# Performance work log

Hardware: AMD Instinct MI355X
Metric: run time of the kernel (lower is better)

## Reference

```python
import jax, jax.numpy as jnp
import numpy as np

NUM_IN_CH = 64
DIM = 256
HEADS = 8


def conv1x1(x, w):
    # x: [b,c,h,w], w: [o,c,1,1] -> [b,o,h,w]
    return jnp.einsum('bchw,oc->bohw', x, w[:, :, 0, 0])


def dwconv3(x, w):
    # depthwise 3x3, padding=1; w: [c,1,3,3]
    return jax.lax.conv_general_dilated(
        x, w, window_strides=(1, 1), padding='SAME',
        feature_group_count=x.shape[1],
        dimension_numbers=('NCHW', 'OIHW', 'NCHW'))


def setup_inputs() -> dict:
    key = jax.random.key(0)
    ks = jax.random.split(key, 12)
    B, C, H, W = 8, NUM_IN_CH, 128, 128
    s = 0.02
    return {
        'x': jax.random.normal(ks[0], (B, C, H, W), jnp.float32),
        'y': jax.random.normal(ks[1], (B, C, H, W), jnp.float32),
        'z': jax.random.normal(ks[2], (B, C, H, W), jnp.float32),
        'Wq': jax.random.normal(ks[3], (DIM, C, 1, 1), jnp.float32) * s,
        'Wq_dw': jax.random.normal(ks[4], (DIM, 1, 3, 3), jnp.float32) * s,
        'Wk': jax.random.normal(ks[5], (DIM, C, 1, 1), jnp.float32) * s,
        'Wk_dw': jax.random.normal(ks[6], (DIM, 1, 3, 3), jnp.float32) * s,
        'Wv': jax.random.normal(ks[7], (DIM, C, 1, 1), jnp.float32) * s,
        'Wv_dw': jax.random.normal(ks[8], (DIM, 1, 3, 3), jnp.float32) * s,
        'Wproj': jax.random.normal(ks[9], (DIM, DIM, 1, 1), jnp.float32) * s,
        'Wfus': jax.random.normal(ks[10], (DIM, 3 * C, 1, 1), jnp.float32) * s,
        'temperature': jnp.ones((HEADS, 1, 1), jnp.float32),
    }


def reference(x, y, z, Wq, Wq_dw, Wk, Wk_dw, Wv, Wv_dw, Wproj, Wfus, temperature):
    b, c, h, w = x.shape
    hw = h * w
    q = dwconv3(conv1x1(x, Wq), Wq_dw)
    k = dwconv3(conv1x1(y, Wk), Wk_dw)
    v = dwconv3(conv1x1(z, Wv), Wv_dw)
    f = conv1x1(jnp.concatenate([x, y, z], axis=1), Wfus)

    def to_heads(t):  # [b, dim, h, w] -> [b, head, c_head, hw]
        return t.reshape(b, HEADS, DIM // HEADS, hw)

    q, k, v = to_heads(q), to_heads(k), to_heads(v)
    # L2-normalize over the spatial (hw) axis, eps matches torch F.normalize
    qn = q / jnp.maximum(jnp.sqrt(jnp.sum(q * q, axis=-1, keepdims=True)), 1e-12)
    kn = k / jnp.maximum(jnp.sqrt(jnp.sum(k * k, axis=-1, keepdims=True)), 1e-12)
    attn = jnp.einsum('bhcn,bhdn->bhcd', qn, kn) * temperature  # [b,head,c,c]
    attn = jax.nn.softmax(attn, axis=-1)
    out = jnp.einsum('bhcd,bhdn->bhcn', attn, v).reshape(b, DIM, h, w)
    out = conv1x1(out, Wproj)
    return out + f
```

## Files before the change

kernel.cpp:

```cpp
#include <hip/hip_runtime.h>
#include <cstdint>

#define B_   8
#define CIN  64
#define DIM_ 256
#define H_   128
#define W_   128
#define HW_  (H_*W_)

typedef unsigned short u16;
typedef unsigned int   u32;
typedef short short8 __attribute__((ext_vector_type(8)));
typedef float f32x4  __attribute__((ext_vector_type(4)));

__device__ __forceinline__ u16 f2bf(float f) {
    u32 u = __float_as_uint(f);
    u32 r = (u + 0x7fffu + ((u >> 16) & 1u)) >> 16;
    return (u16)r;
}
__device__ __forceinline__ float bf2f(u16 h) {
    return __uint_as_float(((u32)h) << 16);
}

__global__ __launch_bounds__(256) void conv_mfma_kernel(
    const float* __restrict__ in, const float* __restrict__ Wc,
    u16* __restrict__ pre)
{
    __shared__ u16 Alds[256 * 64];
    __shared__ u16 Blds[128 * 64];

    const int tid = threadIdx.x;
    const int b = blockIdx.y;
    const int px0 = blockIdx.x * 128;

    {
        const int row = tid;
        const float* wp = Wc + (size_t)row * 64;
        #pragma unroll
        for (int s = 0; s < 8; ++s) {
            float4 f0 = *(const float4*)(wp + s * 8);
            float4 f1 = *(const float4*)(wp + s * 8 + 4);
            uint4 pk;
            pk.x = f2bf(f0.x) | ((u32)f2bf(f0.y) << 16);
            pk.y = f2bf(f0.z) | ((u32)f2bf(f0.w) << 16);
            pk.z = f2bf(f1.x) | ((u32)f2bf(f1.y) << 16);
            pk.w = f2bf(f1.z) | ((u32)f2bf(f1.w) << 16);
            *(uint4*)&Alds[row * 64 + ((s * 8) ^ ((row & 7) << 3))] = pk;
        }
    }
    #pragma unroll
    for (int v4 = 0; v4 < 4; ++v4) {
        int it = tid + v4 * 256;
        int px = it & 127, cg = it >> 7;
        const float* sp = in + ((size_t)b * CIN + cg * 8) * HW_ + px0 + px;
        u32 wv[4];
        #pragma unroll
        for (int j = 0; j < 4; ++j) {
            float a = sp[(size_t)(2 * j) * HW_];
            float c = sp[(size_t)(2 * j + 1) * HW_];
            wv[j] = f2bf(a) | ((u32)f2bf(c) << 16);
        }
        *(uint4*)&Blds[px * 64 + ((cg * 8) ^ ((px & 7) << 3))] =
            make_uint4(wv[0], wv[1], wv[2], wv[3]);
    }
    __syncthreads();

    const int lane = tid & 63, wid = tid >> 6;
    const int g = lane >> 4, ln = lane & 15;
    const int m0 = wid * 64;
    f32x4 acc[4][8] = {};

    #pragma unroll
    for (int ks = 0; ks < 2; ++ks) {
        short8 af[4];
        #pragma unroll
        for (int fm = 0; fm < 4; ++fm) {
            int m = m0 + fm * 16 + ln;
            af[fm] = *(const short8*)&Alds[m * 64 + ((ks * 32 + g * 8) ^ ((m & 7) << 3))];
        }
        #pragma unroll
        for (int fn = 0; fn < 8; ++fn) {
            int p = fn * 16 + ln;
            short8 bf = *(const short8*)&Blds[p * 64 + ((ks * 32 + g * 8) ^ ((p & 7) << 3))];
            #pragma unroll
            for (int fm = 0; fm < 4; ++fm)
                acc[fm][fn] = __builtin_amdgcn_mfma_f32_16x16x32_bf16(af[fm], bf, acc[fm][fn], 0, 0, 0);
        }
    }

    u16* op = pre + (size_t)b * DIM_ * HW_;
    #pragma unroll
    for (int fm = 0; fm < 4; ++fm)
        #pragma unroll
        for (int fn = 0; fn < 8; ++fn)
            #pragma unroll
            for (int r = 0; r < 4; ++r) {
                int ch = m0 + fm * 16 + g * 4 + r;
                op[(size_t)ch * HW_ + px0 + fn * 16 + ln] = f2bf(acc[fm][fn][r]);
            }
}

__global__ __launch_bounds__(256) void dw_kernel(
    const u16* __restrict__ pre, const float* __restrict__ Wd,
    u16* __restrict__ dst)
{
    __shared__ u16 t0[34][144];

    const int tid = threadIdx.x;
    const int y0 = blockIdx.x * 32;
    const int ch = blockIdx.y;
    const int b = blockIdx.z;
    const u16* src = pre + ((size_t)b * DIM_ + ch) * HW_;

    for (int i = tid; i < 68; i += 256)
        t0[i >> 1][(i & 1) ? 136 : 7] = 0;
    for (int i = tid; i < 544; i += 256) {
        int row = i >> 4, seg = i & 15;
        int gy = y0 - 1 + row;
        uint4 v = make_uint4(0, 0, 0, 0);
        if (gy >= 0 && gy < H_) v = *(const uint4*)(src + (size_t)gy * W_ + seg * 8);
        *(uint4*)&t0[row][8 + seg * 8] = v;
    }
    const float* wv = Wd + (size_t)ch * 9;
    float w00 = wv[0], w01 = wv[1], w02 = wv[2];
    float w10 = wv[3], w11 = wv[4], w12 = wv[5];
    float w20 = wv[6], w21 = wv[7], w22 = wv[8];
    __syncthreads();

    const int px = tid & 127, half = tid >> 7;
    u16* op = dst + ((size_t)b * DIM_ + ch) * HW_;
    float h0m2 = 0.f, h0m1 = 0.f, h1m1 = 0.f;
    #pragma unroll
    for (int y = 0; y < 18; ++y) {
        int r = half * 16 + y;
        float v0 = bf2f(t0[r][7 + px]);
        float v1 = bf2f(t0[r][8 + px]);
        float v2 = bf2f(t0[r][9 + px]);
        float h0 = fmaf(v0, w00, fmaf(v1, w01, v2 * w02));
        float h1 = fmaf(v0, w10, fmaf(v1, w11, v2 * w12));
        float h2 = fmaf(v0, w20, fmaf(v1, w21, v2 * w22));
        if (y >= 2)
            op[(size_t)(y0 + half * 16 + y - 2) * W_ + px] = f2bf(h0m2 + h1m1 + h2);
        h0m2 = h0m1; h0m1 = h0; h1m1 = h1;
    }
}

__global__ __launch_bounds__(256) void gram_mfma_kernel(
    const u16* __restrict__ q, const u16* __restrict__ k,
    float* __restrict__ pgram, float* __restrict__ pssq, float* __restrict__ pssk)
{
    __shared__ float red[4][1024];
    __shared__ float redq[4][32];
    __shared__ float redk[4][32];

    const int bh = blockIdx.y;
    const int chunk = blockIdx.x;
    const int tid = threadIdx.x;
    const int lane = tid & 63, wid = tid >> 6;
    const int g = lane >> 4, ln = lane & 15;

    const size_t off = (size_t)(bh * 32 + ln) * HW_ + chunk * 2048 + wid * 512 + g * 8;
    const u16* qp = q + off;
    const u16* kp = k + off;

    f32x4 aqk[2][2] = {};
    f32x4 aqq[2] = {};
    f32x4 akk[2] = {};

    #pragma unroll 4
    for (int n = 0; n < 512; n += 32) {
        short8 qf[2], kf[2];
        qf[0] = *(const short8*)(qp + n);
        qf[1] = *(const short8*)(qp + (size_t)16 * HW_ + n);
        kf[0] = *(const short8*)(kp + n);
        kf[1] = *(const short8*)(kp + (size_t)16 * HW_ + n);
        #pragma unroll
        for (int ti = 0; ti < 2; ++ti)
            #pragma unroll
            for (int tj = 0; tj < 2; ++tj)
                aqk[ti][tj] = __builtin_amdgcn_mfma_f32_16x16x32_bf16(qf[ti], kf[tj], aqk[ti][tj], 0, 0, 0);
        #pragma unroll
        for (int ti = 0; ti < 2; ++ti) {
            aqq[ti] = __builtin_amdgcn_mfma_f32_16x16x32_bf16(qf[ti], qf[ti], aqq[ti], 0, 0, 0);
            akk[ti] = __builtin_amdgcn_mfma_f32_16x16x32_bf16(kf[ti], kf[ti], akk[ti], 0, 0, 0);
        }
    }

    #pragma unroll
    for (int ti = 0; ti < 2; ++ti)
        #pragma unroll
        for (int tj = 0; tj < 2; ++tj)
            #pragma unroll
            for (int r = 0; r < 4; ++r)
                red[wid][(ti * 16 + g * 4 + r) * 32 + tj * 16 + ln] = aqk[ti][tj][r];
    if ((ln >> 2) == g) {
        #pragma unroll
        for (int ti = 0; ti < 2; ++ti) {
            redq[wid][ti * 16 + ln] = aqq[ti][ln & 3];
            redk[wid][ti * 16 + ln] = akk[ti][ln & 3];
        }
    }
    __syncthreads();

    for (int p = tid; p < 1024; p += 256) {
        float s = red[0][p] + red[1][p] + red[2][p] + red[3][p];
        pgram[((size_t)bh * 8 + chunk) * 1024 + p] = s;
    }
    if (tid < 32) {
        pssq[((size_t)bh * 8 + chunk) * 32 + tid] =
            redq[0][tid] + redq[1][tid] + redq[2][tid] + redq[3][tid];
    } else if (tid < 64) {
        int j = tid & 31;
        pssk[((size_t)bh * 8 + chunk) * 32 + j] =
            redk[0][j] + redk[1][j] + redk[2][j] + redk[3][j];
    }
}

__global__ __launch_bounds__(256) void softproj_kernel(
    const float* __restrict__ pgram, const float* __restrict__ pssq,
    const float* __restrict__ pssk, const float* __restrict__ Wproj,
    const float* __restrict__ temp, u16* __restrict__ Amm)
{
    __shared__ float att[32][33];
    __shared__ float nq[32], nk[32];

    const int bh = blockIdx.x;
    const int h = bh & 7;
    const int b = bh >> 3;
    const int tid = threadIdx.x;

    for (int p = tid; p < 1024; p += 256) {
        float s = 0.f;
        #pragma unroll
        for (int c = 0; c < 8; ++c) s += pgram[((size_t)bh * 8 + c) * 1024 + p];
        att[p >> 5][p & 31] = s;
    }
    if (tid < 32) {
        float s = 0.f;
        #pragma unroll
        for (int c = 0; c < 8; ++c) s += pssq[((size_t)bh * 8 + c) * 32 + tid];
        nq[tid] = fmaxf(sqrtf(s), 1e-12f);
    } else if (tid < 64) {
        int i = tid & 31;
        float s = 0.f;
        #pragma unroll
        for (int c = 0; c < 8; ++c) s += pssk[((size_t)bh * 8 + c) * 32 + i];
        nk[i] = fmaxf(sqrtf(s), 1e-12f);
    }
    __syncthreads();

    const float T = temp[h];
    if (tid < 32) {
        int i = tid;
        float row[32];
        float mx = -1e30f;
        float qi = T / nq[i];
        #pragma unroll
        for (int j = 0; j < 32; ++j) {
            float v = att[i][j] * qi / nk[j];
            row[j] = v;
            mx = fmaxf(mx, v);
        }
        float s = 0.f;
        #pragma unroll
        for (int j = 0; j < 32; ++j) { float e = expf(row[j] - mx); row[j] = e; s += e; }
        float inv = 1.f / s;
        #pragma unroll
        for (int j = 0; j < 32; ++j) att[i][j] = row[j] * inv;
    }
    __syncthreads();

    const int o = tid;
    float wp[32];
    #pragma unroll
    for (int i2 = 0; i2 < 32; i2 += 4)
        *(float4*)&wp[i2] = *(const float4*)&Wproj[(size_t)o * DIM_ + h * 32 + i2];
    u16* arow = Amm + ((size_t)b * DIM_ + o) * DIM_ + h * 32;
    #pragma unroll
    for (int j = 0; j < 32; ++j) {
        float s = 0.f;
        #pragma unroll
        for (int i = 0; i < 32; ++i) s = fmaf(wp[i], att[i][j], s);
        arow[j] = f2bf(s);
    }
}

__global__ __launch_bounds__(256) void wfus_cast_kernel(
    const float* __restrict__ Wfus, u16* __restrict__ Afus)
{
    int idx = blockIdx.x * 256 + threadIdx.x;
    int base = idx * 8;
    float4 f0 = *(const float4*)(Wfus + base);
    float4 f1 = *(const float4*)(Wfus + base + 4);
    uint4 pk;
    pk.x = f2bf(f0.x) | ((u32)f2bf(f0.y) << 16);
    pk.y = f2bf(f0.z) | ((u32)f2bf(f0.w) << 16);
    pk.z = f2bf(f1.x) | ((u32)f2bf(f1.y) << 16);
    pk.w = f2bf(f1.z) | ((u32)f2bf(f1.w) << 16);
    *(uint4*)(Afus + base) = pk;
}

#define LOADB_F4(KC, W) do {                                                    \
    if ((KC) < 4) {                                                             \
        _Pragma("unroll") for (int i_ = 0; i_ < 2; ++i_) {                      \
            const u16* vb_ = vbuf + ((size_t)b * DIM_ + (KC) * 64 + (qq0 + 2 * i_) * 16) * HW_ + px0 + pxu; \
            _Pragma("unroll") for (int jj_ = 0; jj_ < 8; ++jj_)                 \
                W[i_][jj_] = (u32)vb_[(size_t)(2 * jj_) * HW_]                  \
                           | ((u32)vb_[(size_t)(2 * jj_ + 1) * HW_] << 16);     \
        }                                                                       \
    } else {                                                                    \
        const float* bp_ = ((KC) == 4) ? xin : ((KC) == 5) ? yin : zin;         \
        _Pragma("unroll") for (int i_ = 0; i_ < 2; ++i_) {                      \
            const float* sp_ = bp_ + ((size_t)b * CIN + (qq0 + 2 * i_) * 16) * HW_ + px0 + pxu; \
            _Pragma("unroll") for (int jj_ = 0; jj_ < 8; ++jj_)                 \
                W[i_][jj_] = (u32)f2bf(sp_[(size_t)(2 * jj_) * HW_])            \
                           | ((u32)f2bf(sp_[(size_t)(2 * jj_ + 1) * HW_]) << 16); \
        }                                                                       \
    } } while (0)

#define WRITEB_F4(BUF, W) do {                                                  \
    u16* dd_ = &Bl[BUF][pxu * 64];                                              \
    _Pragma("unroll") for (int i_ = 0; i_ < 2; ++i_) {                          \
        int qq_ = qq0 + 2 * i_;                                                 \
        *(uint4*)&dd_[(qq_ * 16)     ^ ((pxu & 7) << 3)] = make_uint4(W[i_][0], W[i_][1], W[i_][2], W[i_][3]); \
        *(uint4*)&dd_[(qq_ * 16 + 8) ^ ((pxu & 7) << 3)] = make_uint4(W[i_][4], W[i_][5], W[i_][6], W[i_][7]); \
    } } while (0)

#define LOADA_F4(KC, A) do {                                                    \
    _Pragma("unroll") for (int ks_ = 0; ks_ < 2; ++ks_)                         \
    _Pragma("unroll") for (int fm_ = 0; fm_ < 2; ++fm_) {                       \
        int m_ = m0 + fm_ * 16 + ln;                                            \
        const u16* ap_ = ((KC) < 4)                                             \
            ? Amm + ((size_t)b * DIM_ + m_) * DIM_ + (KC) * 64 + ks_ * 32 + g * 8 \
            : Afus + (size_t)m_ * 192 + ((KC) - 4) * 64 + ks_ * 32 + g * 8;     \
        A[ks_ * 2 + fm_] = *(const short8*)ap_;                                 \
    } } while (0)

__global__ __launch_bounds__(256) void final4_kernel(
    const u16* __restrict__ Amm, const u16* __restrict__ Afus,
    const u16* __restrict__ vbuf,
    const float* __restrict__ xin, const float* __restrict__ yin,
    const float* __restrict__ zin, float* __restrict__ out)
{
    __shared__ u16 Bl[2][128 * 64];

    const int tid = threadIdx.x;
    const int px0 = blockIdx.x * 128;
    const int o0  = blockIdx.y * 128;
    const int b   = blockIdx.z;
    const int lane = tid & 63, wid = tid >> 6;
    const int g = lane >> 4, ln = lane & 15;
    const int m0 = o0 + wid * 32;
    const int pxu = tid & 127;
    const int qq0 = tid >> 7;

    f32x4 acc[2][8] = {};
    short8 aC[4], aN[4];
    u32 wN[2][8];

    LOADA_F4(0, aC);
    {
        u32 w0[2][8];
        LOADB_F4(0, w0);
        WRITEB_F4(0, w0);
    }
    __syncthreads();
    LOADA_F4(1, aN);
    LOADB_F4(1, wN);

    #pragma unroll
    for (int kc = 0; kc < 7; ++kc) {
        const int cur = kc & 1;

        #pragma unroll
        for (int ks = 0; ks < 2; ++ks)
            #pragma unroll
            for (int fn = 0; fn < 8; ++fn) {
                int p = fn * 16 + ln;
                short8 bf = *(const short8*)&Bl[cur][p * 64 + ((ks * 32 + g * 8) ^ ((p & 7) << 3))];
                acc[0][fn] = __builtin_amdgcn_mfma_f32_16x16x32_bf16(aC[ks * 2 + 0], bf, acc[0][fn], 0, 0, 0);
                acc[1][fn] = __builtin_amdgcn_mfma_f32_16x16x32_bf16(aC[ks * 2 + 1], bf, acc[1][fn], 0, 0, 0);
            }

        if (kc < 6) {
            WRITEB_F4(cur ^ 1, wN);
            __syncthreads();
            #pragma unroll
            for (int r = 0; r < 4; ++r) aC[r] = aN[r];
            if (kc < 5) {
                LOADA_F4(kc + 2, aN);
                LOADB_F4(kc + 2, wN);
            }
        }
    }

    float* op = out + (size_t)b * DIM_ * HW_;
    #pragma unroll
    for (int fm = 0; fm < 2; ++fm)
        #pragma unroll
        for (int fn = 0; fn < 8; ++fn)
            #pragma unroll
            for (int r = 0; r < 4; ++r) {
                int ch = m0 + fm * 16 + g * 4 + r;
                op[(size_t)ch * HW_ + px0 + fn * 16 + ln] = acc[fm][fn][r];
            }
}

extern "C" void kernel_launch(void* const* d_in, const int* in_sizes, int n_in,
                              void* d_out, int out_size, void* d_ws, size_t ws_size,
                              hipStream_t stream) {
    (void)in_sizes; (void)n_in; (void)out_size; (void)ws_size;

    const float* x     = (const float*)d_in[0];
    const float* y     = (const float*)d_in[1];
    const float* z     = (const float*)d_in[2];
    const float* Wq    = (const float*)d_in[3];
    const float* Wqd   = (const float*)d_in[4];
    const float* Wk    = (const float*)d_in[5];
    const float* Wkd   = (const float*)d_in[6];
    const float* Wv    = (const float*)d_in[7];
    const float* Wvd   = (const float*)d_in[8];
    const float* Wproj = (const float*)d_in[9];
    const float* Wfus  = (const float*)d_in[10];
    const float* temp  = (const float*)d_in[11];

    const size_t QELEMS = (size_t)B_ * DIM_ * HW_;

    u16* preb = (u16*)d_out;
    u16* qbuf = (u16*)d_out + QELEMS;
    u16* kvbuf = (u16*)d_ws;
    char* wsp = (char*)d_ws + QELEMS * sizeof(u16);
    float* pgram = (float*)wsp;                       wsp += 64 * 8 * 1024 * 4;
    float* pssq  = (float*)wsp;                       wsp += 64 * 8 * 32 * 4;
    float* pssk  = (float*)wsp;                       wsp += 64 * 8 * 32 * 4;
    u16*   Amm   = (u16*)wsp;                         wsp += (size_t)B_ * DIM_ * DIM_ * 2;
    u16*   Afus  = (u16*)wsp;

    dim3 cgrid(128, B_);
    dim3 dgrid(4, DIM_, B_);

    wfus_cast_kernel<<<24, 256, 0, stream>>>(Wfus, Afus);
    conv_mfma_kernel<<<cgrid, 256, 0, stream>>>(x, Wq, preb);
    dw_kernel<<<dgrid, 256, 0, stream>>>(preb, Wqd, qbuf);
    conv_mfma_kernel<<<cgrid, 256, 0, stream>>>(y, Wk, preb);
    dw_kernel<<<dgrid, 256, 0, stream>>>(preb, Wkd, kvbuf);
    gram_mfma_kernel<<<dim3(8, 64), 256, 0, stream>>>(qbuf, kvbuf, pgram, pssq, pssk);
    softproj_kernel<<<64, 256, 0, stream>>>(pgram, pssq, pssk, Wproj, temp, Amm);
    conv_mfma_kernel<<<cgrid, 256, 0, stream>>>(z, Wv, preb);
    dw_kernel<<<dgrid, 256, 0, stream>>>(preb, Wvd, kvbuf);
    final4_kernel<<<dim3(128, 2, B_), 256, 0, stream>>>(Amm, Afus, kvbuf, x, y, z, (float*)d_out);
}
```

Baseline: 289.8 us.

## Store V path in pixel-major layout so final GEMM reads B fragments directly

Adds a V 1x1 conv kernel that transposes its output through LDS into pixel-major (channel-contiguous) layout. It also adds a depthwise conv kernel that works on that layout with vectorized channel loads. The final GEMM then loads the V operand fragments straight from global memory as short8 vectors, instead of gathering strided bf16 values and staging them in LDS. This is meant to remove uncoalesced 2-byte gathers. The cost is an extra LDS transpose pass and a dwconv that re-reads neighbours from global memory without LDS tiling.

```diff
diff --git a/kernel.cpp b/kernel.cpp
--- a/kernel.cpp
+++ b/kernel.cpp
@@ -98,6 +98,100 @@
                 int ch = m0 + fm * 16 + g * 4 + r;
                 op[(size_t)ch * HW_ + px0 + fn * 16 + ln] = f2bf(acc[fm][fn][r]);
             }
+}
+
+__global__ __launch_bounds__(256) void conv_mfma_t_kernel(
+    const float* __restrict__ in, const float* __restrict__ Wc,
+    u16* __restrict__ preT)
+{
+    __shared__ u16 S[128 * 264];
+
+    u16* Alds = S;
+    u16* Blds = S + 16384;
+
+    const int tid = threadIdx.x;
+    const int b = blockIdx.y;
+    const int px0 = blockIdx.x * 128;
+
+    {
+        const int row = tid;
+        const float* wp = Wc + (size_t)row * 64;
+        #pragma unroll
+        for (int s = 0; s < 8; ++s) {
+            float4 f0 = *(const float4*)(wp + s * 8);
+            float4 f1 = *(const float4*)(wp + s * 8 + 4);
+            uint4 pk;
+            pk.x = f2bf(f0.x) | ((u32)f2bf(f0.y) << 16);
+            pk.y = f2bf(f0.z) | ((u32)f2bf(f0.w) << 16);
+            pk.z = f2bf(f1.x) | ((u32)f2bf(f1.y) << 16);
+            pk.w = f2bf(f1.z) | ((u32)f2bf(f1.w) << 16);
+            *(uint4*)&Alds[row * 64 + ((s * 8) ^ ((row & 7) << 3))] = pk;
+        }
+    }
+    #pragma unroll
+    for (int v4 = 0; v4 < 4; ++v4) {
+        int it = tid + v4 * 256;
+        int px = it & 127, cg = it >> 7;
+        const float* sp = in + ((size_t)b * CIN + cg * 8) * HW_ + px0 + px;
+        u32 wv[4];
+        #pragma unroll
+        for (int j = 0; j < 4; ++j) {
+            float a = sp[(size_t)(2 * j) * HW_];
+            float c = sp[(size_t)(2 * j + 1) * HW_];
+            wv[j] = f2bf(a) | ((u32)f2bf(c) << 16);
+        }
+        *(uint4*)&Blds[px * 64 + ((cg * 8) ^ ((px & 7) << 3))] =
+            make_uint4(wv[0], wv[1], wv[2], wv[3]);
+    }
+    __syncthreads();
+
+    const int lane = tid & 63, wid = tid >> 6;
+    const int g = lane >> 4, ln = lane & 15;
+    const int m0 = wid * 64;
+    f32x4 acc[4][8] = {};
+
+    #pragma unroll
+    for (int ks = 0; ks < 2; ++ks) {
+        short8 af[4];
+        #pragma unroll
+        for (int fm = 0; fm < 4; ++fm) {
+            int m = m0 + fm * 16 + ln;
+            af[fm] = *(const short8*)&Alds[m * 64 + ((ks * 32 + g * 8) ^ ((m & 7) << 3))];
+        }
+        #pragma unroll
+        for (int fn = 0; fn < 8; ++fn) {
+            int p = fn * 16 + ln;
+            short8 bf = *(const short8*)&Blds[p * 64 + ((ks * 32 + g * 8) ^ ((p & 7) << 3))];
+            #pragma unroll
+            for (int fm = 0; fm < 4; ++fm)
+                acc[fm][fn] = __builtin_amdgcn_mfma_f32_16x16x32_bf16(af[fm], bf, acc[fm][fn], 0, 0, 0);
+        }
+    }
+    __syncthreads();
+
+    #pragma unroll
+    for (int fm = 0; fm < 4; ++fm)
+        #pragma unroll
+        for (int fn = 0; fn < 8; ++fn) {
+            int px = fn * 16 + ln;
+            int ch0 = m0 + fm * 16 + g * 4;
+            int idx = px * 264 + ((ch0 + 8 * ((px >> 3) & 7)) & 255);
+            u32 a0 = f2bf(acc[fm][fn][0]) | ((u32)f2bf(acc[fm][fn][1]) << 16);
+            u32 a1 = f2bf(acc[fm][fn][2]) | ((u32)f2bf(acc[fm][fn][3]) << 16);
+            *(uint2*)&S[idx] = make_uint2(a0, a1);
+        }
+    __syncthreads();
+
+    {
+        int px = tid >> 1, half = tid & 1;
+        int rot = 8 * ((px >> 3) & 7);
+        u16* dst = preT + ((size_t)b * HW_ + px0 + px) * 256 + half * 128;
+        #pragma unroll
+        for (int s = 0; s < 16; ++s) {
+            int ch = half * 128 + s * 8;
+            *(uint4*)(dst + s * 8) = *(const uint4*)&S[px * 264 + ((ch + rot) & 255)];
+        }
+    }
 }
 
 __global__ __launch_bounds__(256) void dw_kernel(
@@ -145,6 +239,73 @@
     }
 }
 
+__global__ __launch_bounds__(256) void dwt_kernel(
+    const u16* __restrict__ preT, const float* __restrict__ Wd,
+    u16* __restrict__ vT)
+{
+    __shared__ float wlds[9 * 260];
+
+    const int tid = threadIdx.x;
+    const int y = blockIdx.x;
+    const int b = blockIdx.y;
+
+    for (int i = tid; i < 2304; i += 256) {
+        int o = i % 9, ch = i / 9;
+        wlds[o * 260 + ch] = Wd[(size_t)ch * 9 + o];
+    }
+    __syncthreads();
+
+    const int ch0 = (tid & 31) * 8;
+    const int xg = tid >> 5;
+    const u16* base = preT + (size_t)b * HW_ * 256;
+
+    #pragma unroll
+    for (int blk = 0; blk < 4; ++blk) {
+        const int x0 = xg * 16 + blk * 4;
+        float acc[4][8] = {};
+        #pragma unroll
+        for (int dy = -1; dy <= 1; ++dy) {
+            int row = y + dy;
+            if (row < 0 || row >= H_) continue;
+            float vf[6][8];
+            #pragma unroll
+            for (int c = 0; c < 6; ++c) {
+                int xx = x0 - 1 + c;
+                uint4 raw = make_uint4(0, 0, 0, 0);
+                if (xx >= 0 && xx < W_)
+                    raw = *(const uint4*)(base + ((size_t)row * W_ + xx) * 256 + ch0);
+                #pragma unroll
+                for (int e = 0; e < 4; ++e) {
+                    u32 w = ((const u32*)&raw)[e];
+                    vf[c][2 * e]     = __uint_as_float(w << 16);
+                    vf[c][2 * e + 1] = __uint_as_float(w & 0xffff0000u);
+                }
+            }
+            #pragma unroll
+            for (int dx = 0; dx < 3; ++dx) {
+                int o = (dy + 1) * 3 + dx;
+                float4 w0 = *(const float4*)&wlds[o * 260 + ch0];
+                float4 w1 = *(const float4*)&wlds[o * 260 + ch0 + 4];
+                float ww[8] = {w0.x, w0.y, w0.z, w0.w, w1.x, w1.y, w1.z, w1.w};
+                #pragma unroll
+                for (int xi = 0; xi < 4; ++xi)
+                    #pragma unroll
+                    for (int j = 0; j < 8; ++j)
+                        acc[xi][j] = fmaf(ww[j], vf[xi + dx][j], acc[xi][j]);
+            }
+        }
+        #pragma unroll
+        for (int xi = 0; xi < 4; ++xi) {
+            uint4 pk;
+            pk.x = f2bf(acc[xi][0]) | ((u32)f2bf(acc[xi][1]) << 16);
+            pk.y = f2bf(acc[xi][2]) | ((u32)f2bf(acc[xi][3]) << 16);
+            pk.z = f2bf(acc[xi][4]) | ((u32)f2bf(acc[xi][5]) << 16);
+            pk.w = f2bf(acc[xi][6]) | ((u32)f2bf(acc[xi][7]) << 16);
+            *(uint4*)(vT + ((size_t)b * HW_ + (size_t)y * W_ + x0 + xi) * 256 + ch0) = pk;
+        }
+    }
+}
+
 __global__ __launch_bounds__(256) void gram_mfma_kernel(
     const u16* __restrict__ q, const u16* __restrict__ k,
     float* __restrict__ pgram, float* __restrict__ pssq, float* __restrict__ pssk)
@@ -300,25 +461,16 @@
     *(uint4*)(Afus + base) = pk;
 }
 
-#define LOADB_F4(KC, W) do {                                                    \
-    if ((KC) < 4) {                                                             \
-        _Pragma("unroll") for (int i_ = 0; i_ < 2; ++i_) {                      \
-            const u16* vb_ = vbuf + ((size_t)b * DIM_ + (KC) * 64 + (qq0 + 2 * i_) * 16) * HW_ + px0 + pxu; \
-            _Pragma("unroll") for (int jj_ = 0; jj_ < 8; ++jj_)                 \
-                W[i_][jj_] = (u32)vb_[(size_t)(2 * jj_) * HW_]                  \
-                           | ((u32)vb_[(size_t)(2 * jj_ + 1) * HW_] << 16);     \
-        }                                                                       \
-    } else {                                                                    \
-        const float* bp_ = ((KC) == 4) ? xin : ((KC) == 5) ? yin : zin;         \
-        _Pragma("unroll") for (int i_ = 0; i_ < 2; ++i_) {                      \
-            const float* sp_ = bp_ + ((size_t)b * CIN + (qq0 + 2 * i_) * 16) * HW_ + px0 + pxu; \
-            _Pragma("unroll") for (int jj_ = 0; jj_ < 8; ++jj_)                 \
-                W[i_][jj_] = (u32)f2bf(sp_[(size_t)(2 * jj_) * HW_])            \
-                           | ((u32)f2bf(sp_[(size_t)(2 * jj_ + 1) * HW_]) << 16); \
-        }                                                                       \
+#define LOADBX_F5(KC, W) do {                                                   \
+    const float* bp_ = ((KC) == 4) ? xin : ((KC) == 5) ? yin : zin;             \
+    _Pragma("unroll") for (int i_ = 0; i_ < 2; ++i_) {                          \
+        const float* sp_ = bp_ + ((size_t)b * CIN + (qq0 + 2 * i_) * 16) * HW_ + px0 + pxu; \
+        _Pragma("unroll") for (int jj_ = 0; jj_ < 8; ++jj_)                     \
+            W[i_][jj_] = (u32)f2bf(sp_[(size_t)(2 * jj_) * HW_])                \
+                       | ((u32)f2bf(sp_[(size_t)(2 * jj_ + 1) * HW_]) << 16);   \
     } } while (0)
 
-#define WRITEB_F4(BUF, W) do {                                                  \
+#define WRITEB_F5(BUF, W) do {                                                  \
     u16* dd_ = &Bl[BUF][pxu * 64];                                              \
     _Pragma("unroll") for (int i_ = 0; i_ < 2; ++i_) {                          \
         int qq_ = qq0 + 2 * i_;                                                 \
@@ -326,7 +478,7 @@
         *(uint4*)&dd_[(qq_ * 16 + 8) ^ ((pxu & 7) << 3)] = make_uint4(W[i_][4], W[i_][5], W[i_][6], W[i_][7]); \
     } } while (0)
 
-#define LOADA_F4(KC, A) do {                                                    \
+#define LOADA_F5(KC, A) do {                                                    \
     _Pragma("unroll") for (int ks_ = 0; ks_ < 2; ++ks_)                         \
     _Pragma("unroll") for (int fm_ = 0; fm_ < 2; ++fm_) {                       \
         int m_ = m0 + fm_ * 16 + ln;                                            \
@@ -336,9 +488,9 @@
         A[ks_ * 2 + fm_] = *(const short8*)ap_;                                 \
     } } while (0)
 
-__global__ __launch_bounds__(256) void final4_kernel(
+__global__ __launch_bounds__(256) void final5_kernel(
     const u16* __restrict__ Amm, const u16* __restrict__ Afus,
-    const u16* __restrict__ vbuf,
+    const u16* __restrict__ vT,
     const float* __restrict__ xin, const float* __restrict__ yin,
     const float* __restrict__ zin, float* __restrict__ out)
 {
@@ -355,23 +507,37 @@
     const int qq0 = tid >> 7;
 
     f32x4 acc[2][8] = {};
+
+    const u16* vrow = vT + ((size_t)b * HW_ + px0 + ln) * 256 + g * 8;
+    #pragma unroll
+    for (int kc = 0; kc < 4; ++kc) {
+        short8 a[4];
+        LOADA_F5(kc, a);
+        #pragma unroll
+        for (int ks = 0; ks < 2; ++ks)
+            #pragma unroll
+            for (int fn = 0; fn < 8; ++fn) {
+                short8 bf = *(const short8*)(vrow + (size_t)(fn * 16) * 256 + kc * 64 + ks * 32);
+                acc[0][fn] = __builtin_amdgcn_mfma_f32_16x16x32_bf16(a[ks * 2 + 0], bf, acc[0][fn], 0, 0, 0);
+                acc[1][fn] = __builtin_amdgcn_mfma_f32_16x16x32_bf16(a[ks * 2 + 1], bf, acc[1][fn], 0, 0, 0);
+            }
+    }
+
     short8 aC[4], aN[4];
     u32 wN[2][8];
-
-    LOADA_F4(0, aC);
+    LOADA_F5(4, aC);
     {
         u32 w0[2][8];
-        LOADB_F4(0, w0);
-        WRITEB_F4(0, w0);
-    }
-    __syncthreads();
-    LOADA_F4(1, aN);
-    LOADB_F4(1, wN);
-
-    #pragma unroll
-    for (int kc = 0; kc < 7; ++kc) {
+        LOADBX_F5(4, w0);
+        WRITEB_F5(0, w0);
+    }
+    __syncthreads();
+    LOADA_F5(5, aN);
+    LOADBX_F5(5, wN);
+
+    #pragma unroll
+    for (int kc = 4; kc < 7; ++kc) {
         const int cur = kc & 1;
-
         #pragma unroll
         for (int ks = 0; ks < 2; ++ks)
             #pragma unroll
@@ -381,15 +547,14 @@
                 acc[0][fn] = __builtin_amdgcn_mfma_f32_16x16x32_bf16(aC[ks * 2 + 0], bf, acc[0][fn], 0, 0, 0);
                 acc[1][fn] = __builtin_amdgcn_mfma_f32_16x16x32_bf16(aC[ks * 2 + 1], bf, acc[1][fn], 0, 0, 0);
             }
-
         if (kc < 6) {
-            WRITEB_F4(cur ^ 1, wN);
+            WRITEB_F5(cur ^ 1, wN);
             __syncthreads();
             #pragma unroll
             for (int r = 0; r < 4; ++r) aC[r] = aN[r];
             if (kc < 5) {
-                LOADA_F4(kc + 2, aN);
-                LOADB_F4(kc + 2, wN);
+                LOADA_F5(6, aN);
+                LOADBX_F5(6, wN);
             }
         }
     }
@@ -446,7 +611,7 @@
     dw_kernel<<<dgrid, 256, 0, stream>>>(preb, Wkd, kvbuf);
     gram_mfma_kernel<<<dim3(8, 64), 256, 0, stream>>>(qbuf, kvbuf, pgram, pssq, pssk);
     softproj_kernel<<<64, 256, 0, stream>>>(pgram, pssq, pssk, Wproj, temp, Amm);
-    conv_mfma_kernel<<<cgrid, 256, 0, stream>>>(z, Wv, preb);
-    dw_kernel<<<dgrid, 256, 0, stream>>>(preb, Wvd, kvbuf);
-    final4_kernel<<<dim3(128, 2, B_), 256, 0, stream>>>(Amm, Afus, kvbuf, x, y, z, (float*)d_out);
-}
+    conv_mfma_t_kernel<<<cgrid, 256, 0, stream>>>(z, Wv, preb);
+    dwt_kernel<<<dim3(128, B_), 256, 0, stream>>>(preb, Wvd, kvbuf);
+    final5_kernel<<<dim3(128, 2, B_), 256, 0, stream>>>(Amm, Afus, kvbuf, x, y, z, (float*)d_out);
+}
```

Measured after the change: 404.0 us. 1.39x slower.
